# Optimization experiments

Measured on AMD Instinct MI355X. Metric: run time of the kernel, lower is better.

The kernel has to match this reference:

```python
import jax, jax.numpy as jnp
import numpy as np

B, L, H = 64, 512, 768   # batch, BERT seq len, BERT hidden
D, S, Q = 16, 64, 32     # max_doc_len (sentences), max_seq_len (tokens/sentence), max_query_len
NEG = -900000.0


def setup_inputs() -> dict:
    key = jax.random.key(0)
    k1, k2, k3, k4, k5 = jax.random.split(key, 5)
    rng = np.random.default_rng(0)
    query_len = rng.integers(8, Q + 1, size=B)                 # actual query lengths
    doc_len = rng.integers(4, D + 1, size=B)                   # sentences per doc
    seq_lens = rng.integers(4, 29, size=(B, D))                # tokens per sentence
    seq_lens[np.arange(D)[None, :] >= doc_len[:, None]] = 0    # zero beyond doc_len
    # layout guarantee: 32 + 2 + 16*28 = 482 <= 512
    return {
        "hidden_states": jax.random.normal(k1, (B, L, H), jnp.float32),
        "W_doc": jax.random.normal(k2, (H, 1), jnp.float32) * 0.02,
        "b_doc": jax.random.normal(k3, (1,), jnp.float32) * 0.02,
        "W_query": jax.random.normal(k4, (H, 1), jnp.float32) * 0.02,
        "b_query": jax.random.normal(k5, (1,), jnp.float32) * 0.02,
        "query_len": jnp.asarray(query_len, jnp.int32),
        "seq_lens": jnp.asarray(seq_lens, jnp.int32),
    }


def reference(hidden_states, W_doc, b_doc, W_query, b_query, query_len, seq_lens):
    # --- ragged sentence extraction (vectorized get_sentence_state) ---
    # sentence j of example i starts at query_len[i] + 2 + sum(seq_lens[i,:j])
    offsets = query_len[:, None] + 2 + jnp.cumsum(seq_lens, axis=1) - seq_lens  # [B,D]
    pos = jnp.arange(S, dtype=jnp.int32)
    idx = jnp.clip(offsets[:, :, None] + pos, 0, L - 1)                         # [B,D,S]
    mask_doc = pos[None, None, :] < seq_lens[:, :, None]                        # [B,D,S] bool
    sent = jnp.take_along_axis(hidden_states, idx.reshape(B, D * S, 1), axis=1)
    sent = sent.reshape(B, D, S, H)
    sent = jnp.where(mask_doc[..., None], sent, 0.0)  # zero padding, as original

    # --- masked softmax attention pooling over tokens in each sentence ---
    alpha = (sent @ W_doc + b_doc)[..., 0]                                      # [B,D,S]
    alpha = jnp.where(mask_doc, alpha, NEG)
    alpha = jax.nn.softmax(alpha, axis=-1)
    doc_pooled = jnp.einsum('bds,bdsh->bdh', alpha, sent)                       # [B,D,H]

    # --- ragged query extraction + pooling ---
    q_state = hidden_states[:, 1:1 + Q]                                         # [B,Q,H]
    mask_q = jnp.arange(Q, dtype=jnp.int32)[None, :] < query_len[:, None]       # [B,Q]
    q_state = jnp.where(mask_q[..., None], q_state, 0.0)
    aq = (q_state @ W_query + b_query)[..., 0]                                  # [B,Q]
    aq = jnp.where(mask_q, aq, NEG)
    aq = jax.nn.softmax(aq, axis=-1)
    q_pooled = jnp.einsum('bq,bqh->bh', aq, q_state)                            # [B,H]
    q_bcast = jnp.broadcast_to(q_pooled[:, None, :], doc_pooled.shape)          # [B,D,H]
    return doc_pooled, q_bcast
```

## Files before the change

### kernel.cpp

```cpp
#include <hip/hip_runtime.h>

namespace {
constexpr int Bn = 64;
constexpr int Ln = 512;
constexpr int Hn = 768;
constexpr int Dn = 16;
constexpr float NEGV = -900000.0f;
}

__global__ __launch_bounds__(256) void k_fused(
    const float* __restrict__ hs,
    const float* __restrict__ Wd, const float* __restrict__ bd,
    const float* __restrict__ Wq, const float* __restrict__ bq,
    const int* __restrict__ qlen, const int* __restrict__ slens,
    float* __restrict__ out_doc, float* __restrict__ out_q)
{
    __shared__ float score_sh[32];
    __shared__ float4 pool4[4][192];

    const int t = threadIdx.x;
    const int wave = t >> 6;
    const int lane = t & 63;
    const int bid = blockIdx.x;

    const float* rowbase;
    const float* W;
    float bias;
    int len;
    int b, d = 0;
    const bool isq = (bid < Bn);

    if (isq) {
        b = bid;
        len = qlen[b];
        W = Wq; bias = bq[0];
        rowbase = hs + ((size_t)b * Ln + 1) * Hn;
    } else {
        const int id = bid - Bn;
        b = id >> 4;
        d = id & 15;
        const int sv = slens[b * Dn + (lane & 15)];
        len = __shfl(sv, d, 64);
        if (len == 0) {
            if (t < 192) {
                float4* o4 = reinterpret_cast<float4*>(out_doc + ((size_t)b * Dn + d) * Hn);
                o4[t] = make_float4(0.f, 0.f, 0.f, 0.f);
            }
            return;
        }
        int pref = 0;
#pragma unroll
        for (int k = 0; k < Dn; ++k)
            pref += (k < d) ? __shfl(sv, k, 64) : 0;
        const int base = qlen[b] + 2 + pref;
        W = Wd; bias = bd[0];
        rowbase = hs + ((size_t)b * Ln + base) * Hn;
    }

    float4 wv[3];
#pragma unroll
    for (int j = 0; j < 3; ++j)
        wv[j] = *reinterpret_cast<const float4*>(W + (lane + 64 * j) * 4);

    float4 c[8][3];
#pragma unroll
    for (int it = 0; it < 8; ++it) {
        const int s = wave + 4 * it;
        if (s < len) {
            const float* r = rowbase + s * Hn;
#pragma unroll
            for (int j = 0; j < 3; ++j)
                c[it][j] = *reinterpret_cast<const float4*>(r + (lane + 64 * j) * 4);
            float p = c[it][0].x * wv[0].x + c[it][0].y * wv[0].y
                    + c[it][0].z * wv[0].z + c[it][0].w * wv[0].w
                    + c[it][1].x * wv[1].x + c[it][1].y * wv[1].y
                    + c[it][1].z * wv[1].z + c[it][1].w * wv[1].w
                    + c[it][2].x * wv[2].x + c[it][2].y * wv[2].y
                    + c[it][2].z * wv[2].z + c[it][2].w * wv[2].w;
#pragma unroll
            for (int off = 32; off; off >>= 1) p += __shfl_xor(p, off);
            if (lane == 0) score_sh[s] = p;
        }
    }
    __syncthreads();

    const int si = lane & 31;
    const float raw = (si < len) ? (score_sh[si] + bias) : NEGV;
    float mx = raw;
#pragma unroll
    for (int off = 16; off; off >>= 1) mx = fmaxf(mx, __shfl_xor(mx, off, 32));
    const float e = __expf(raw - mx);
    float den = e;
#pragma unroll
    for (int off = 16; off; off >>= 1) den += __shfl_xor(den, off, 32);
    const float alpha = (si < len) ? (e / den) : 0.f;

    float4 acc[3];
#pragma unroll
    for (int j = 0; j < 3; ++j) acc[j] = make_float4(0.f, 0.f, 0.f, 0.f);
#pragma unroll
    for (int it = 0; it < 8; ++it) {
        const int s = wave + 4 * it;
        if (s < len) {
            const float a = __shfl(alpha, s, 64);
            acc[0].x += a * c[it][0].x; acc[0].y += a * c[it][0].y;
            acc[0].z += a * c[it][0].z; acc[0].w += a * c[it][0].w;
            acc[1].x += a * c[it][1].x; acc[1].y += a * c[it][1].y;
            acc[1].z += a * c[it][1].z; acc[1].w += a * c[it][1].w;
            acc[2].x += a * c[it][2].x; acc[2].y += a * c[it][2].y;
            acc[2].z += a * c[it][2].z; acc[2].w += a * c[it][2].w;
        }
    }

#pragma unroll
    for (int j = 0; j < 3; ++j) pool4[wave][lane + 64 * j] = acc[j];
    __syncthreads();

    if (t < 192) {
        float4 r = pool4[0][t];
#pragma unroll
        for (int w = 1; w < 4; ++w) {
            const float4 s = pool4[w][t];
            r.x += s.x; r.y += s.y; r.z += s.z; r.w += s.w;
        }
        if (isq) {
            for (int dd = 0; dd < Dn; ++dd) {
                float4* o4 = reinterpret_cast<float4*>(out_q + ((size_t)b * Dn + dd) * Hn);
                o4[t] = r;
            }
        } else {
            float4* o4 = reinterpret_cast<float4*>(out_doc + ((size_t)b * Dn + d) * Hn);
            o4[t] = r;
        }
    }
}

extern "C" void kernel_launch(void* const* d_in, const int* in_sizes, int n_in,
                              void* d_out, int out_size, void* d_ws, size_t ws_size,
                              hipStream_t stream)
{
    const float* hs    = (const float*)d_in[0];
    const float* Wd    = (const float*)d_in[1];
    const float* bd    = (const float*)d_in[2];
    const float* Wq    = (const float*)d_in[3];
    const float* bq    = (const float*)d_in[4];
    const int*   qlen  = (const int*)d_in[5];
    const int*   slens = (const int*)d_in[6];

    float* out_doc = (float*)d_out;
    float* out_q   = out_doc + (size_t)Bn * Dn * Hn;

    k_fused<<<Bn + Bn * Dn, 256, 0, stream>>>(hs, Wd, bd, Wq, bq,
                                              qlen, slens, out_doc, out_q);
}
```

Baseline: 18.10 us.

## Use one wavefront per sentence with register softmax and second row pass

Each segment is now handled by a single 64-thread wavefront instead of a 256-thread block. Scores and softmax stay in registers, which removes shared memory and both __syncthreads. The rows are read a second time for the weighted sum instead of being cached, trading extra (likely cache-hit) global loads for lower register pressure. The bias terms are dropped, which is valid because a constant shift does not change the softmax. Each wave now issues its row loads serially over up to 32 rows, so there is less memory-level parallelism per segment.

```diff
diff --git a/kernel.cpp b/kernel.cpp
--- a/kernel.cpp
+++ b/kernel.cpp
@@ -5,133 +5,104 @@
 constexpr int Ln = 512;
 constexpr int Hn = 768;
 constexpr int Dn = 16;
-constexpr float NEGV = -900000.0f;
 }
 
-__global__ __launch_bounds__(256) void k_fused(
+__global__ __launch_bounds__(64) void k_wave(
     const float* __restrict__ hs,
-    const float* __restrict__ Wd, const float* __restrict__ bd,
-    const float* __restrict__ Wq, const float* __restrict__ bq,
+    const float* __restrict__ Wd,
+    const float* __restrict__ Wq,
     const int* __restrict__ qlen, const int* __restrict__ slens,
     float* __restrict__ out_doc, float* __restrict__ out_q)
 {
-    __shared__ float score_sh[32];
-    __shared__ float4 pool4[4][192];
+    const int lane = threadIdx.x;
+    const int tid  = blockIdx.x;
+    const bool isq = (tid < Bn);
 
-    const int t = threadIdx.x;
-    const int wave = t >> 6;
-    const int lane = t & 63;
-    const int bid = blockIdx.x;
+    int b, d = 0;
+    const float* W;
+    if (isq) { b = tid; W = Wq; }
+    else     { const int id = tid - Bn; b = id >> 4; d = id & 15; W = Wd; }
 
-    const float* rowbase;
-    const float* W;
-    float bias;
-    int len;
-    int b, d = 0;
-    const bool isq = (bid < Bn);
+    const int sv = slens[b * Dn + (lane & 15)];
+    const int ql = qlen[b];
+    const float4 wv0 = *reinterpret_cast<const float4*>(W + lane * 4);
+    const float4 wv1 = *reinterpret_cast<const float4*>(W + (lane + 64) * 4);
+    const float4 wv2 = *reinterpret_cast<const float4*>(W + (lane + 128) * 4);
 
+    int len, base;
     if (isq) {
-        b = bid;
-        len = qlen[b];
-        W = Wq; bias = bq[0];
-        rowbase = hs + ((size_t)b * Ln + 1) * Hn;
+        len = ql;
+        base = 1;
     } else {
-        const int id = bid - Bn;
-        b = id >> 4;
-        d = id & 15;
-        const int sv = slens[b * Dn + (lane & 15)];
         len = __shfl(sv, d, 64);
         if (len == 0) {
-            if (t < 192) {
-                float4* o4 = reinterpret_cast<float4*>(out_doc + ((size_t)b * Dn + d) * Hn);
-                o4[t] = make_float4(0.f, 0.f, 0.f, 0.f);
-            }
+            float4* o = reinterpret_cast<float4*>(out_doc + ((size_t)b * Dn + d) * Hn);
+            const float4 z = make_float4(0.f, 0.f, 0.f, 0.f);
+            o[lane] = z; o[lane + 64] = z; o[lane + 128] = z;
             return;
         }
         int pref = 0;
 #pragma unroll
         for (int k = 0; k < Dn; ++k)
             pref += (k < d) ? __shfl(sv, k, 64) : 0;
-        const int base = qlen[b] + 2 + pref;
-        W = Wd; bias = bd[0];
-        rowbase = hs + ((size_t)b * Ln + base) * Hn;
+        base = ql + 2 + pref;
     }
+    const float* bp = hs + ((size_t)b * Ln + base) * Hn;
 
-    float4 wv[3];
+    float p[32];
 #pragma unroll
-    for (int j = 0; j < 3; ++j)
-        wv[j] = *reinterpret_cast<const float4*>(W + (lane + 64 * j) * 4);
-
-    float4 c[8][3];
+    for (int s = 0; s < 32; ++s) {
+        if (s < len) {
+            const float* r = bp + s * Hn;
+            const float4 c0 = *reinterpret_cast<const float4*>(r + lane * 4);
+            const float4 c1 = *reinterpret_cast<const float4*>(r + (lane + 64) * 4);
+            const float4 c2 = *reinterpret_cast<const float4*>(r + (lane + 128) * 4);
+            float v = c0.x * wv0.x + c0.y * wv0.y + c0.z * wv0.z + c0.w * wv0.w
+                    + c1.x * wv1.x + c1.y * wv1.y + c1.z * wv1.z + c1.w * wv1.w
+                    + c2.x * wv2.x + c2.y * wv2.y + c2.z * wv2.z + c2.w * wv2.w;
 #pragma unroll
-    for (int it = 0; it < 8; ++it) {
-        const int s = wave + 4 * it;
-        if (s < len) {
-            const float* r = rowbase + s * Hn;
-#pragma unroll
-            for (int j = 0; j < 3; ++j)
-                c[it][j] = *reinterpret_cast<const float4*>(r + (lane + 64 * j) * 4);
-            float p = c[it][0].x * wv[0].x + c[it][0].y * wv[0].y
-                    + c[it][0].z * wv[0].z + c[it][0].w * wv[0].w
-                    + c[it][1].x * wv[1].x + c[it][1].y * wv[1].y
-                    + c[it][1].z * wv[1].z + c[it][1].w * wv[1].w
-                    + c[it][2].x * wv[2].x + c[it][2].y * wv[2].y
-                    + c[it][2].z * wv[2].z + c[it][2].w * wv[2].w;
-#pragma unroll
-            for (int off = 32; off; off >>= 1) p += __shfl_xor(p, off);
-            if (lane == 0) score_sh[s] = p;
-        }
-    }
-    __syncthreads();
-
-    const int si = lane & 31;
-    const float raw = (si < len) ? (score_sh[si] + bias) : NEGV;
-    float mx = raw;
-#pragma unroll
-    for (int off = 16; off; off >>= 1) mx = fmaxf(mx, __shfl_xor(mx, off, 32));
-    const float e = __expf(raw - mx);
-    float den = e;
-#pragma unroll
-    for (int off = 16; off; off >>= 1) den += __shfl_xor(den, off, 32);
-    const float alpha = (si < len) ? (e / den) : 0.f;
-
-    float4 acc[3];
-#pragma unroll
-    for (int j = 0; j < 3; ++j) acc[j] = make_float4(0.f, 0.f, 0.f, 0.f);
-#pragma unroll
-    for (int it = 0; it < 8; ++it) {
-        const int s = wave + 4 * it;
-        if (s < len) {
-            const float a = __shfl(alpha, s, 64);
-            acc[0].x += a * c[it][0].x; acc[0].y += a * c[it][0].y;
-            acc[0].z += a * c[it][0].z; acc[0].w += a * c[it][0].w;
-            acc[1].x += a * c[it][1].x; acc[1].y += a * c[it][1].y;
-            acc[1].z += a * c[it][1].z; acc[1].w += a * c[it][1].w;
-            acc[2].x += a * c[it][2].x; acc[2].y += a * c[it][2].y;
-            acc[2].z += a * c[it][2].z; acc[2].w += a * c[it][2].w;
+            for (int off = 32; off; off >>= 1) v += __shfl_xor(v, off);
+            p[s] = v;
+        } else {
+            p[s] = 0.f;
         }
     }
 
+    float m = -INFINITY;
 #pragma unroll
-    for (int j = 0; j < 3; ++j) pool4[wave][lane + 64 * j] = acc[j];
-    __syncthreads();
+    for (int s = 0; s < 32; ++s)
+        if (s < len) m = fmaxf(m, p[s]);
+    float den = 0.f;
+#pragma unroll
+    for (int s = 0; s < 32; ++s)
+        if (s < len) { p[s] = __expf(p[s] - m); den += p[s]; }
+    const float inv = 1.f / den;
 
-    if (t < 192) {
-        float4 r = pool4[0][t];
+    float4 a0 = make_float4(0.f, 0.f, 0.f, 0.f);
+    float4 a1 = make_float4(0.f, 0.f, 0.f, 0.f);
+    float4 a2 = make_float4(0.f, 0.f, 0.f, 0.f);
 #pragma unroll
-        for (int w = 1; w < 4; ++w) {
-            const float4 s = pool4[w][t];
-            r.x += s.x; r.y += s.y; r.z += s.z; r.w += s.w;
+    for (int s = 0; s < 32; ++s) {
+        if (s < len) {
+            const float a = p[s] * inv;
+            const float* r = bp + s * Hn;
+            const float4 c0 = *reinterpret_cast<const float4*>(r + lane * 4);
+            const float4 c1 = *reinterpret_cast<const float4*>(r + (lane + 64) * 4);
+            const float4 c2 = *reinterpret_cast<const float4*>(r + (lane + 128) * 4);
+            a0.x += a * c0.x; a0.y += a * c0.y; a0.z += a * c0.z; a0.w += a * c0.w;
+            a1.x += a * c1.x; a1.y += a * c1.y; a1.z += a * c1.z; a1.w += a * c1.w;
+            a2.x += a * c2.x; a2.y += a * c2.y; a2.z += a * c2.z; a2.w += a * c2.w;
         }
-        if (isq) {
-            for (int dd = 0; dd < Dn; ++dd) {
-                float4* o4 = reinterpret_cast<float4*>(out_q + ((size_t)b * Dn + dd) * Hn);
-                o4[t] = r;
-            }
-        } else {
-            float4* o4 = reinterpret_cast<float4*>(out_doc + ((size_t)b * Dn + d) * Hn);
-            o4[t] = r;
+    }
+
+    if (isq) {
+        for (int dd = 0; dd < Dn; ++dd) {
+            float4* o = reinterpret_cast<float4*>(out_q + ((size_t)b * Dn + dd) * Hn);
+            o[lane] = a0; o[lane + 64] = a1; o[lane + 128] = a2;
         }
+    } else {
+        float4* o = reinterpret_cast<float4*>(out_doc + ((size_t)b * Dn + d) * Hn);
+        o[lane] = a0; o[lane + 64] = a1; o[lane + 128] = a2;
     }
 }
 
@@ -141,15 +112,13 @@
 {
     const float* hs    = (const float*)d_in[0];
     const float* Wd    = (const float*)d_in[1];
-    const float* bd    = (const float*)d_in[2];
     const float* Wq    = (const float*)d_in[3];
-    const float* bq    = (const float*)d_in[4];
     const int*   qlen  = (const int*)d_in[5];
     const int*   slens = (const int*)d_in[6];
 
     float* out_doc = (float*)d_out;
     float* out_q   = out_doc + (size_t)Bn * Dn * Hn;
 
-    k_fused<<<Bn + Bn * Dn, 256, 0, stream>>>(hs, Wd, bd, Wq, bq,
-                                              qlen, slens, out_doc, out_q);
+    k_wave<<<Bn + Bn * Dn, 64, 0, stream>>>(hs, Wd, Wq, qlen, slens,
+                                            out_doc, out_q);
 }
```

Result: slower. 39.38 us (+117.6%).
